# Kernel optimization log

Measured on AMD Instinct MI355X. Metric: run time of the kernel, lower is better.

The kernel has to match this reference:

```python
import jax, jax.numpy as jnp
import numpy as np

EMBED_DIM = 1024
NUM_HEADS = 16
HEAD_DIM = EMBED_DIM // NUM_HEADS
BATCH = 2
SEQ = 2048


def setup_inputs() -> dict:
    key = jax.random.key(0)
    ks = jax.random.split(key, 9)
    s = EMBED_DIM ** -0.5
    inp = {"x": jax.random.normal(ks[0], (BATCH, SEQ, EMBED_DIM), dtype=jnp.float32)}
    names = ["Wq", "Wk", "Wv", "Wo"]
    for i, n in enumerate(names):
        inp[n] = jax.random.normal(ks[1 + i], (EMBED_DIM, EMBED_DIM), dtype=jnp.float32) * s
        inp["b" + n[1]] = jax.random.normal(ks[5 + i], (EMBED_DIM,), dtype=jnp.float32) * 0.02
    return inp


def reference(x, Wq, bq, Wk, bk, Wv, bv, Wo, bo):
    B, S, E = x.shape
    H, D = NUM_HEADS, HEAD_DIM
    scaling = D ** -0.5
    # projections (torch Linear: x @ W.T + b), reshape to (B, H, S, D)
    q = (x @ Wq.T + bq).reshape(B, S, H, D).transpose(0, 2, 1, 3)
    k = (x @ Wk.T + bk).reshape(B, S, H, D).transpose(0, 2, 1, 3)
    v = (x @ Wv.T + bv).reshape(B, S, H, D).transpose(0, 2, 1, 3)
    # full materialized score matrix, matching the original module
    scores = jnp.einsum("bhqd,bhkd->bhqk", q, k) * scaling
    causal = jnp.triu(jnp.ones((S, S), dtype=bool), k=1)  # True above diagonal
    scores = jnp.where(causal[None, None], -jnp.inf, scores)
    attn = jax.nn.softmax(scores, axis=-1)
    out = jnp.einsum("bhqk,bhkd->bhqd", attn, v)  # (B, H, S, D)
    out = out.transpose(0, 2, 1, 3).reshape(B, S, E)
    return out @ Wo.T + bo
```

## Files before the change

kernel.cpp:

```cpp
#include <hip/hip_runtime.h>
#include <stdint.h>

typedef __bf16 bf16;
typedef __bf16 bf16x8 __attribute__((ext_vector_type(8)));
typedef __bf16 bf16x4 __attribute__((ext_vector_type(4)));
typedef float  f32x4  __attribute__((ext_vector_type(4)));

#define E_DIM 1024
#define S_LEN 2048
#define BATCH 2
#define NH 16
#define DH 64

#define NEG_INF (-__builtin_inff())

__device__ __forceinline__ void load_lds16(const bf16* g, bf16* l) {
    __builtin_amdgcn_global_load_lds(
        (const __attribute__((address_space(1))) void*)g,
        (__attribute__((address_space(3))) void*)l, 16, 0, 0);
}

__global__ __launch_bounds__(256) void convert_kernel(
    const float* __restrict__ s0, const float* __restrict__ s1,
    const float* __restrict__ s2, const float* __restrict__ s3,
    const float* __restrict__ s4,
    bf16* __restrict__ d0, bf16* __restrict__ d1, bf16* __restrict__ d2,
    bf16* __restrict__ d3, bf16* __restrict__ d4,
    int n0, int n1)
{
    const float* src; bf16* dst; int n;
    switch (blockIdx.y) {
        case 0:  src = s0; dst = d0; n = n0; break;
        case 1:  src = s1; dst = d1; n = n1; break;
        case 2:  src = s2; dst = d2; n = n1; break;
        case 3:  src = s3; dst = d3; n = n1; break;
        default: src = s4; dst = d4; n = n1; break;
    }
    int i = (blockIdx.x * 256 + threadIdx.x) * 4;
    if (i >= n) return;
    float4 v = *(const float4*)(src + i);
    bf16x4 o;
    o[0] = (bf16)v.x; o[1] = (bf16)v.y; o[2] = (bf16)v.z; o[3] = (bf16)v.w;
    *(bf16x4*)(dst + i) = o;
}

__global__ __launch_bounds__(256) void gemm_kernel(
    const bf16* __restrict__ A,
    const bf16* __restrict__ W0, const bf16* __restrict__ W1, const bf16* __restrict__ W2,
    const float* __restrict__ bias0, const float* __restrict__ bias1, const float* __restrict__ bias2,
    bf16* __restrict__ outQ, bf16* __restrict__ outK, bf16* __restrict__ outVt,
    float* __restrict__ outF, int final_mode)
{
    __shared__ bf16 As0[128 * 32], As1[128 * 32];
    __shared__ bf16 Bs0[128 * 32], Bs1[128 * 32];

    int mode;
    const bf16* W; const float* bias;
    if (final_mode) { mode = 3; W = W0; bias = bias0; }
    else {
        mode = blockIdx.z;
        W    = (mode == 0) ? W0 : (mode == 1 ? W1 : W2);
        bias = (mode == 0) ? bias0 : (mode == 1 ? bias1 : bias2);
    }

    const int bm = blockIdx.y * 128, bn = blockIdx.x * 128;
    const int t = threadIdx.x;
    const int lane = t & 63, w = t >> 6;
    const int quad = lane >> 4, l16 = lane & 15;
    const int wm = (w & 1) * 64, wn = (w >> 1) * 64;

    const int r0 = w * 16;
    const int srow = r0 + (lane >> 2), scol = (lane & 3) * 8;
    const bf16* Ag0 = A + (size_t)(bm + srow) * E_DIM + scol;
    const bf16* Ag1 = Ag0 + (size_t)64 * E_DIM;
    const bf16* Wg0 = W + (size_t)(bn + srow) * E_DIM + scol;
    const bf16* Wg1 = Wg0 + (size_t)64 * E_DIM;
    bf16* a00 = As0 + r0 * 32;  bf16* a01 = As0 + (64 + r0) * 32;
    bf16* a10 = As1 + r0 * 32;  bf16* a11 = As1 + (64 + r0) * 32;
    bf16* b00 = Bs0 + r0 * 32;  bf16* b01 = Bs0 + (64 + r0) * 32;
    bf16* b10 = Bs1 + r0 * 32;  bf16* b11 = Bs1 + (64 + r0) * 32;

    f32x4 acc[4][4];
#pragma unroll
    for (int i = 0; i < 4; i++)
#pragma unroll
        for (int j = 0; j < 4; j++) acc[i][j] = f32x4{0.f, 0.f, 0.f, 0.f};

    for (int kt = 0; kt < E_DIM; kt += 64) {
        __syncthreads();
        load_lds16(Ag0 + kt,      a00);
        load_lds16(Ag1 + kt,      a01);
        load_lds16(Ag0 + kt + 32, a10);
        load_lds16(Ag1 + kt + 32, a11);
        load_lds16(Wg0 + kt,      b00);
        load_lds16(Wg1 + kt,      b01);
        load_lds16(Wg0 + kt + 32, b10);
        load_lds16(Wg1 + kt + 32, b11);
        __syncthreads();

#pragma unroll
        for (int half = 0; half < 2; half++) {
            const bf16* Asx = half ? As1 : As0;
            const bf16* Bsx = half ? Bs1 : Bs0;
            bf16x8 af[4], bfr[4];
#pragma unroll
            for (int i = 0; i < 4; i++)
                af[i] = *(const bf16x8*)(Asx + (wm + i * 16 + l16) * 32 + quad * 8);
#pragma unroll
            for (int j = 0; j < 4; j++)
                bfr[j] = *(const bf16x8*)(Bsx + (wn + j * 16 + l16) * 32 + quad * 8);
#pragma unroll
            for (int i = 0; i < 4; i++)
#pragma unroll
                for (int j = 0; j < 4; j++)
                    acc[i][j] = __builtin_amdgcn_mfma_f32_16x16x32_bf16(af[i], bfr[j], acc[i][j], 0, 0, 0);
        }
    }

#pragma unroll
    for (int j = 0; j < 4; j++) {
        const int n = bn + wn + j * 16 + l16;
        const float bv = bias[n];
#pragma unroll
        for (int i = 0; i < 4; i++) {
            const int m0 = bm + wm + i * 16 + quad * 4;
            if (mode == 3) {
#pragma unroll
                for (int r = 0; r < 4; r++)
                    outF[(size_t)(m0 + r) * E_DIM + n] = acc[i][j][r] + bv;
            } else if (mode == 2) {
                const int b_ = m0 >> 11, s0 = m0 & (S_LEN - 1);
                const int h = n >> 6, d = n & 63;
                bf16x4 pv;
#pragma unroll
                for (int r = 0; r < 4; r++) pv[r] = (bf16)(acc[i][j][r] + bv);
                *(bf16x4*)(outVt + ((size_t)((b_ * NH + h) * DH + d)) * S_LEN + s0) = pv;
            } else {
                bf16* o = (mode == 0) ? outQ : outK;
                const float sc = (mode == 0) ? 0.125f : 1.0f;
                const int h = n >> 6, d = n & 63;
#pragma unroll
                for (int r = 0; r < 4; r++) {
                    const int m = m0 + r;
                    const int b_ = m >> 11, s = m & (S_LEN - 1);
                    o[((size_t)(b_ * NH + h) * S_LEN + s) * DH + d] = (bf16)((acc[i][j][r] + bv) * sc);
                }
            }
        }
    }
}

__global__ __launch_bounds__(256, 2) void attn_kernel(
    const bf16* __restrict__ Qb, const bf16* __restrict__ Kb,
    const bf16* __restrict__ Vtb, bf16* __restrict__ Ob)
{
    __shared__ bf16 Ks[128 * 72];
    __shared__ bf16 Vs[64 * 136];
    __shared__ bf16 Ps[4][16 * 136];

    const int t = threadIdx.x, lane = t & 63, w = t >> 6;
    const int quad = lane >> 4, l16 = lane & 15;

    const int i = blockIdx.x;
    const int xcd = i & 7, rr = i >> 3;
    const int bh = (xcd << 2) | (rr & 3);
    const int pr = rr >> 2;
    const int qtl = pr, qth = 31 - pr;

    const bf16* Qg = Qb + (size_t)bh * S_LEN * DH;
    const bf16* Kg = Kb + (size_t)bh * S_LEN * DH;
    const bf16* Vg = Vtb + (size_t)bh * DH * S_LEN;
    const int b_ = bh >> 4, h = bh & 15;
    bf16* Og = Ob + (size_t)b_ * S_LEN * E_DIM + h * DH;

    bf16* Pw = Ps[w];

    bf16x8 aq[2][2];
#pragma unroll
    for (int qt = 0; qt < 2; qt++) {
        const int qrow0 = (qt ? qth : qtl) * 64 + w * 16;
        const bf16* qp = Qg + (size_t)(qrow0 + l16) * DH + quad * 8;
        aq[qt][0] = *(const bf16x8*)(qp);
        aq[qt][1] = *(const bf16x8*)(qp + 32);
    }

    f32x4 o[2][4];
    float l_part[2][4];
#pragma unroll
    for (int qt = 0; qt < 2; qt++)
#pragma unroll
        for (int dt = 0; dt < 4; dt++) {
            o[qt][dt] = f32x4{0.f, 0.f, 0.f, 0.f};
            l_part[qt][dt] = 0.f;
        }

    const int nkt_lo = (qtl >> 1) + 1;
    const int T = (qth >> 1) + 1;
    const int krow = t >> 3, kcol8 = (t & 7) * 8;
    const int vrow = t >> 4, vcol8 = (t & 15) * 8;

    uint4 kc[4], vc[4];
#pragma unroll
    for (int k = 0; k < 4; k++)
        kc[k] = *(const uint4*)(Kg + (size_t)(krow + 32 * k) * DH + kcol8);
#pragma unroll
    for (int k = 0; k < 4; k++)
        vc[k] = *(const uint4*)(Vg + (size_t)(vrow + 16 * k) * S_LEN + vcol8);

    for (int kt = 0; kt < T; kt++) {
        __syncthreads();
#pragma unroll
        for (int k = 0; k < 4; k++)
            *(uint4*)(Ks + (krow + 32 * k) * 72 + kcol8) = kc[k];
#pragma unroll
        for (int k = 0; k < 4; k++)
            *(uint4*)(Vs + (vrow + 16 * k) * 136 + vcol8) = vc[k];
        __syncthreads();

        if (kt + 1 < T) {
            const int nb = (kt + 1) * 128;
#pragma unroll
            for (int k = 0; k < 4; k++)
                kc[k] = *(const uint4*)(Kg + (size_t)(nb + krow + 32 * k) * DH + kcol8);
#pragma unroll
            for (int k = 0; k < 4; k++)
                vc[k] = *(const uint4*)(Vg + (size_t)(vrow + 16 * k) * S_LEN + nb + vcol8);
        }

#pragma unroll
        for (int qt = 0; qt < 2; qt++) {
            if (qt == 0 && kt >= nkt_lo) continue;
            const int qtile = qt ? qth : qtl;
            const bool diag = (kt == (qtile >> 1));

            f32x4 sv[8];
#pragma unroll
            for (int jt = 0; jt < 8; jt++) {
                const bf16* kp = Ks + (jt * 16 + l16) * 72 + quad * 8;
                bf16x8 bk0 = *(const bf16x8*)(kp);
                bf16x8 bk1 = *(const bf16x8*)(kp + 32);
                f32x4 s = f32x4{0.f, 0.f, 0.f, 0.f};
                s = __builtin_amdgcn_mfma_f32_16x16x32_bf16(aq[qt][0], bk0, s, 0, 0, 0);
                s = __builtin_amdgcn_mfma_f32_16x16x32_bf16(aq[qt][1], bk1, s, 0, 0, 0);
                sv[jt] = s;
            }

            if (diag) {
                const int inrow_base = 64 * (qtile & 1) + w * 16 + quad * 4;
#pragma unroll
                for (int jt = 0; jt < 8; jt++) {
                    const int kcol = jt * 16 + l16;
#pragma unroll
                    for (int r = 0; r < 4; r++)
                        if (kcol > inrow_base + r) sv[jt][r] = NEG_INF;
                }
            }

#pragma unroll
            for (int jt = 0; jt < 8; jt++)
#pragma unroll
                for (int r = 0; r < 4; r++) {
                    const float pe = __expf(sv[jt][r]);
                    sv[jt][r] = pe;
                    l_part[qt][r] += pe;
                }

#pragma unroll
            for (int jt = 0; jt < 8; jt++)
#pragma unroll
                for (int r = 0; r < 4; r++)
                    Pw[(quad * 4 + r) * 136 + jt * 16 + l16] = (bf16)sv[jt][r];

#pragma unroll
            for (int ks = 0; ks < 4; ks++) {
                bf16x8 ap = *(const bf16x8*)(Pw + l16 * 136 + ks * 32 + quad * 8);
#pragma unroll
                for (int dt = 0; dt < 4; dt++) {
                    bf16x8 bv = *(const bf16x8*)(Vs + (dt * 16 + l16) * 136 + ks * 32 + quad * 8);
                    o[qt][dt] = __builtin_amdgcn_mfma_f32_16x16x32_bf16(ap, bv, o[qt][dt], 0, 0, 0);
                }
            }
        }
    }

#pragma unroll
    for (int qt = 0; qt < 2; qt++) {
        const int qrow0 = (qt ? qth : qtl) * 64 + w * 16;
#pragma unroll
        for (int r = 0; r < 4; r++) {
            float l = l_part[qt][r];
            l += __shfl_xor(l, 1);
            l += __shfl_xor(l, 2);
            l += __shfl_xor(l, 4);
            l += __shfl_xor(l, 8);
            l_part[qt][r] = 1.0f / l;
        }
#pragma unroll
        for (int r = 0; r < 4; r++) {
            const int srow = qrow0 + quad * 4 + r;
#pragma unroll
            for (int dt = 0; dt < 4; dt++)
                Og[(size_t)srow * E_DIM + dt * 16 + l16] =
                    (bf16)(o[qt][dt][r] * l_part[qt][r]);
        }
    }
}

extern "C" void kernel_launch(void* const* d_in, const int* in_sizes, int n_in,
                              void* d_out, int out_size, void* d_ws, size_t ws_size,
                              hipStream_t stream)
{
    const float* x  = (const float*)d_in[0];
    const float* Wq = (const float*)d_in[1];
    const float* bq = (const float*)d_in[2];
    const float* Wk = (const float*)d_in[3];
    const float* bk = (const float*)d_in[4];
    const float* Wv = (const float*)d_in[5];
    const float* bv = (const float*)d_in[6];
    const float* Wo = (const float*)d_in[7];
    const float* bo = (const float*)d_in[8];
    float* out = (float*)d_out;

    char* ws = (char*)d_ws;
    const size_t MB = 1ull << 20;
    bf16* xb  = (bf16*)(ws + 0);
    bf16* wqb = (bf16*)(ws + 8 * MB);
    bf16* wkb = (bf16*)(ws + 10 * MB);
    bf16* wvb = (bf16*)(ws + 12 * MB);
    bf16* wob = (bf16*)(ws + 14 * MB);
    bf16* Qb  = (bf16*)(ws + 16 * MB);
    bf16* Kb  = (bf16*)(ws + 24 * MB);
    bf16* Vtb = (bf16*)(ws + 32 * MB);
    bf16* Ab  = (bf16*)(ws + 40 * MB);

    convert_kernel<<<dim3(4096, 5), 256, 0, stream>>>(
        x, Wq, Wk, Wv, Wo, xb, wqb, wkb, wvb, wob, 4194304, 1048576);

    gemm_kernel<<<dim3(8, 32, 3), 256, 0, stream>>>(
        xb, wqb, wkb, wvb, bq, bk, bv, Qb, Kb, Vtb, nullptr, 0);

    attn_kernel<<<dim3(512), 256, 0, stream>>>(Qb, Kb, Vtb, Ab);

    gemm_kernel<<<dim3(8, 32, 1), 256, 0, stream>>>(
        Ab, wob, wob, wob, bo, bo, bo, nullptr, nullptr, nullptr, out, 1);
}
```

Baseline: 239.9 us.

## Double-buffer GEMM LDS tiles and enlarge attention blocks to 128-row query tiles

The projection GEMM now steps K by 32 with two LDS buffers. It issues the next tile's global-to-LDS loads before computing on the current one, so each step needs one barrier instead of two. The attention kernel moves to 512-thread blocks with 8 waves covering 128-row query tiles, and launches 256 blocks instead of 512. Masking, exp and P stores are fused into the QK loop. The register prefetch of the next K/V tile is dropped in favour of loading right before the barrier. This may expose global load latency, and halving the block count leaves roughly one block per CU.

```diff
diff --git a/kernel.cpp b/kernel.cpp
--- a/kernel.cpp
+++ b/kernel.cpp
@@ -51,8 +51,8 @@
     bf16* __restrict__ outQ, bf16* __restrict__ outK, bf16* __restrict__ outVt,
     float* __restrict__ outF, int final_mode)
 {
-    __shared__ bf16 As0[128 * 32], As1[128 * 32];
-    __shared__ bf16 Bs0[128 * 32], Bs1[128 * 32];
+    __shared__ bf16 As[2][128 * 32];
+    __shared__ bf16 Bs[2][128 * 32];
 
     int mode;
     const bf16* W; const float* bias;
@@ -75,10 +75,6 @@
     const bf16* Ag1 = Ag0 + (size_t)64 * E_DIM;
     const bf16* Wg0 = W + (size_t)(bn + srow) * E_DIM + scol;
     const bf16* Wg1 = Wg0 + (size_t)64 * E_DIM;
-    bf16* a00 = As0 + r0 * 32;  bf16* a01 = As0 + (64 + r0) * 32;
-    bf16* a10 = As1 + r0 * 32;  bf16* a11 = As1 + (64 + r0) * 32;
-    bf16* b00 = Bs0 + r0 * 32;  bf16* b01 = Bs0 + (64 + r0) * 32;
-    bf16* b10 = Bs1 + r0 * 32;  bf16* b11 = Bs1 + (64 + r0) * 32;
 
     f32x4 acc[4][4];
 #pragma unroll
@@ -86,35 +82,37 @@
 #pragma unroll
         for (int j = 0; j < 4; j++) acc[i][j] = f32x4{0.f, 0.f, 0.f, 0.f};
 
-    for (int kt = 0; kt < E_DIM; kt += 64) {
+    load_lds16(Ag0, As[0] + r0 * 32);
+    load_lds16(Ag1, As[0] + (64 + r0) * 32);
+    load_lds16(Wg0, Bs[0] + r0 * 32);
+    load_lds16(Wg1, Bs[0] + (64 + r0) * 32);
+
+    int cur = 0;
+    for (int kt = 0; kt < E_DIM; kt += 32) {
         __syncthreads();
-        load_lds16(Ag0 + kt,      a00);
-        load_lds16(Ag1 + kt,      a01);
-        load_lds16(Ag0 + kt + 32, a10);
-        load_lds16(Ag1 + kt + 32, a11);
-        load_lds16(Wg0 + kt,      b00);
-        load_lds16(Wg1 + kt,      b01);
-        load_lds16(Wg0 + kt + 32, b10);
-        load_lds16(Wg1 + kt + 32, b11);
-        __syncthreads();
-
-#pragma unroll
-        for (int half = 0; half < 2; half++) {
-            const bf16* Asx = half ? As1 : As0;
-            const bf16* Bsx = half ? Bs1 : Bs0;
-            bf16x8 af[4], bfr[4];
-#pragma unroll
-            for (int i = 0; i < 4; i++)
-                af[i] = *(const bf16x8*)(Asx + (wm + i * 16 + l16) * 32 + quad * 8);
+
+        if (kt + 32 < E_DIM) {
+            const int nxt = cur ^ 1;
+            load_lds16(Ag0 + kt + 32, As[nxt] + r0 * 32);
+            load_lds16(Ag1 + kt + 32, As[nxt] + (64 + r0) * 32);
+            load_lds16(Wg0 + kt + 32, Bs[nxt] + r0 * 32);
+            load_lds16(Wg1 + kt + 32, Bs[nxt] + (64 + r0) * 32);
+        }
+
+        bf16x8 af[4], bfr[4];
+#pragma unroll
+        for (int i = 0; i < 4; i++)
+            af[i] = *(const bf16x8*)(As[cur] + (wm + i * 16 + l16) * 32 + quad * 8);
+#pragma unroll
+        for (int j = 0; j < 4; j++)
+            bfr[j] = *(const bf16x8*)(Bs[cur] + (wn + j * 16 + l16) * 32 + quad * 8);
+#pragma unroll
+        for (int i = 0; i < 4; i++)
 #pragma unroll
             for (int j = 0; j < 4; j++)
-                bfr[j] = *(const bf16x8*)(Bsx + (wn + j * 16 + l16) * 32 + quad * 8);
-#pragma unroll
-            for (int i = 0; i < 4; i++)
-#pragma unroll
-                for (int j = 0; j < 4; j++)
-                    acc[i][j] = __builtin_amdgcn_mfma_f32_16x16x32_bf16(af[i], bfr[j], acc[i][j], 0, 0, 0);
-        }
+                acc[i][j] = __builtin_amdgcn_mfma_f32_16x16x32_bf16(af[i], bfr[j], acc[i][j], 0, 0, 0);
+
+        cur ^= 1;
     }
 
 #pragma unroll
@@ -150,13 +148,13 @@
     }
 }
 
-__global__ __launch_bounds__(256, 2) void attn_kernel(
+__global__ __launch_bounds__(512, 2) void attn_kernel(
     const bf16* __restrict__ Qb, const bf16* __restrict__ Kb,
     const bf16* __restrict__ Vtb, bf16* __restrict__ Ob)
 {
     __shared__ bf16 Ks[128 * 72];
     __shared__ bf16 Vs[64 * 136];
-    __shared__ bf16 Ps[4][16 * 136];
+    __shared__ bf16 Ps[8][16 * 136];
 
     const int t = threadIdx.x, lane = t & 63, w = t >> 6;
     const int quad = lane >> 4, l16 = lane & 15;
@@ -165,7 +163,7 @@
     const int xcd = i & 7, rr = i >> 3;
     const int bh = (xcd << 2) | (rr & 3);
     const int pr = rr >> 2;
-    const int qtl = pr, qth = 31 - pr;
+    const int qlo = pr, qhi = 15 - pr;
 
     const bf16* Qg = Qb + (size_t)bh * S_LEN * DH;
     const bf16* Kg = Kb + (size_t)bh * S_LEN * DH;
@@ -174,11 +172,12 @@
     bf16* Og = Ob + (size_t)b_ * S_LEN * E_DIM + h * DH;
 
     bf16* Pw = Ps[w];
+    const int inrow0 = w * 16;
 
     bf16x8 aq[2][2];
 #pragma unroll
     for (int qt = 0; qt < 2; qt++) {
-        const int qrow0 = (qt ? qth : qtl) * 64 + w * 16;
+        const int qrow0 = (qt ? qhi : qlo) * 128 + inrow0;
         const bf16* qp = Qg + (size_t)(qrow0 + l16) * DH + quad * 8;
         aq[qt][0] = *(const bf16x8*)(qp);
         aq[qt][1] = *(const bf16x8*)(qp + 32);
@@ -194,46 +193,29 @@
             l_part[qt][dt] = 0.f;
         }
 
-    const int nkt_lo = (qtl >> 1) + 1;
-    const int T = (qth >> 1) + 1;
-    const int krow = t >> 3, kcol8 = (t & 7) * 8;
-    const int vrow = t >> 4, vcol8 = (t & 15) * 8;
-
-    uint4 kc[4], vc[4];
-#pragma unroll
-    for (int k = 0; k < 4; k++)
-        kc[k] = *(const uint4*)(Kg + (size_t)(krow + 32 * k) * DH + kcol8);
-#pragma unroll
-    for (int k = 0; k < 4; k++)
-        vc[k] = *(const uint4*)(Vg + (size_t)(vrow + 16 * k) * S_LEN + vcol8);
+    const int T = qhi + 1;
+    const int kr0 = t >> 3, kce = (t & 7) * 8;
+    const int vr0 = t >> 4, vce = (t & 15) * 8;
 
     for (int kt = 0; kt < T; kt++) {
+        const int kb = kt * 128;
+        uint4 k0 = *(const uint4*)(Kg + (size_t)(kb + kr0) * DH + kce);
+        uint4 k1 = *(const uint4*)(Kg + (size_t)(kb + kr0 + 64) * DH + kce);
+        uint4 v0 = *(const uint4*)(Vg + (size_t)vr0 * S_LEN + kb + vce);
+        uint4 v1 = *(const uint4*)(Vg + (size_t)(vr0 + 32) * S_LEN + kb + vce);
         __syncthreads();
-#pragma unroll
-        for (int k = 0; k < 4; k++)
-            *(uint4*)(Ks + (krow + 32 * k) * 72 + kcol8) = kc[k];
-#pragma unroll
-        for (int k = 0; k < 4; k++)
-            *(uint4*)(Vs + (vrow + 16 * k) * 136 + vcol8) = vc[k];
+        *(uint4*)(Ks + kr0 * 72 + kce) = k0;
+        *(uint4*)(Ks + (kr0 + 64) * 72 + kce) = k1;
+        *(uint4*)(Vs + vr0 * 136 + vce) = v0;
+        *(uint4*)(Vs + (vr0 + 32) * 136 + vce) = v1;
         __syncthreads();
 
-        if (kt + 1 < T) {
-            const int nb = (kt + 1) * 128;
-#pragma unroll
-            for (int k = 0; k < 4; k++)
-                kc[k] = *(const uint4*)(Kg + (size_t)(nb + krow + 32 * k) * DH + kcol8);
-#pragma unroll
-            for (int k = 0; k < 4; k++)
-                vc[k] = *(const uint4*)(Vg + (size_t)(vrow + 16 * k) * S_LEN + nb + vcol8);
-        }
-
 #pragma unroll
         for (int qt = 0; qt < 2; qt++) {
-            if (qt == 0 && kt >= nkt_lo) continue;
-            const int qtile = qt ? qth : qtl;
-            const bool diag = (kt == (qtile >> 1));
-
-            f32x4 sv[8];
+            if (qt == 0 && kt > qlo) continue;
+            const bool diag = qt ? (kt == qhi) : (kt == qlo);
+            const int irb = inrow0 + quad * 4;
+
 #pragma unroll
             for (int jt = 0; jt < 8; jt++) {
                 const bf16* kp = Ks + (jt * 16 + l16) * 72 + quad * 8;
@@ -242,34 +224,16 @@
                 f32x4 s = f32x4{0.f, 0.f, 0.f, 0.f};
                 s = __builtin_amdgcn_mfma_f32_16x16x32_bf16(aq[qt][0], bk0, s, 0, 0, 0);
                 s = __builtin_amdgcn_mfma_f32_16x16x32_bf16(aq[qt][1], bk1, s, 0, 0, 0);
-                sv[jt] = s;
-            }
-
-            if (diag) {
-                const int inrow_base = 64 * (qtile & 1) + w * 16 + quad * 4;
-#pragma unroll
-                for (int jt = 0; jt < 8; jt++) {
-                    const int kcol = jt * 16 + l16;
-#pragma unroll
-                    for (int r = 0; r < 4; r++)
-                        if (kcol > inrow_base + r) sv[jt][r] = NEG_INF;
+                const int kcol = jt * 16 + l16;
+#pragma unroll
+                for (int r = 0; r < 4; r++) {
+                    float sval = s[r];
+                    if (diag && kcol > irb + r) sval = NEG_INF;
+                    const float pe = __expf(sval);
+                    l_part[qt][r] += pe;
+                    Pw[(quad * 4 + r) * 136 + jt * 16 + l16] = (bf16)pe;
                 }
             }
-
-#pragma unroll
-            for (int jt = 0; jt < 8; jt++)
-#pragma unroll
-                for (int r = 0; r < 4; r++) {
-                    const float pe = __expf(sv[jt][r]);
-                    sv[jt][r] = pe;
-                    l_part[qt][r] += pe;
-                }
-
-#pragma unroll
-            for (int jt = 0; jt < 8; jt++)
-#pragma unroll
-                for (int r = 0; r < 4; r++)
-                    Pw[(quad * 4 + r) * 136 + jt * 16 + l16] = (bf16)sv[jt][r];
 
 #pragma unroll
             for (int ks = 0; ks < 4; ks++) {
@@ -285,7 +249,7 @@
 
 #pragma unroll
     for (int qt = 0; qt < 2; qt++) {
-        const int qrow0 = (qt ? qth : qtl) * 64 + w * 16;
+        const int qrow0 = (qt ? qhi : qlo) * 128 + inrow0;
 #pragma unroll
         for (int r = 0; r < 4; r++) {
             float l = l_part[qt][r];
@@ -339,7 +303,7 @@
     gemm_kernel<<<dim3(8, 32, 3), 256, 0, stream>>>(
         xb, wqb, wkb, wvb, bq, bk, bv, Qb, Kb, Vtb, nullptr, 0);
 
-    attn_kernel<<<dim3(512), 256, 0, stream>>>(Qb, Kb, Vtb, Ab);
+    attn_kernel<<<dim3(256), 512, 0, stream>>>(Qb, Kb, Vtb, Ab);
 
     gemm_kernel<<<dim3(8, 32, 1), 256, 0, stream>>>(
         Ab, wob, wob, wob, bo, bo, bo, nullptr, nullptr, nullptr, out, 1);
```

Result: faster. 197.8 us (-17.5%).
